# Performance work log

Hardware: AMD Instinct MI355X
Metric: run time of the kernel (lower is better)

Reference implementation:

```python
import jax, jax.numpy as jnp
import numpy as np

B, N, O, K, F = 4, 256, 5, 5, 256
H, D, DFF = 4, 64, 1024  # num_heads, KQ_len, FFN hidden
EPS = 1e-5


def setup_inputs() -> dict:
    key = jax.random.key(0)
    ks = jax.random.split(key, 16)
    s = 0.05
    p = lambda k, shape: (jax.random.normal(k, shape, jnp.float32) * s)
    return {
        "x": jax.random.normal(ks[0], (B, N, O, K, K, F), jnp.float32),
        "Wq": p(ks[1], (H * D, F)), "bq": p(ks[2], (H * D,)),
        "Wk": p(ks[3], (H * D, F)), "bk": p(ks[4], (H * D,)),
        "Wv": p(ks[5], (H * D, F)), "bv": p(ks[6], (H * D,)),
        "Wf": p(ks[7], (F, F)), "bf": p(ks[8], (F,)),
        "ln1_w": jnp.ones((N, O, F), jnp.float32), "ln1_b": jnp.zeros((N, O, F), jnp.float32),
        "ln2_w": jnp.ones((N, O, F), jnp.float32), "ln2_b": jnp.zeros((N, O, F), jnp.float32),
        "W1": p(ks[9], (DFF, F)), "b1": p(ks[10], (DFF,)),
        "W2": p(ks[11], (F, DFF)), "b2": p(ks[12], (F,)),
    }


def _layer_norm3(x, w, b):
    # torch LayerNorm with normalized_shape=[N, O, F]: stats over last 3 dims
    mu = jnp.mean(x, axis=(1, 2, 3), keepdims=True)
    var = jnp.var(x, axis=(1, 2, 3), keepdims=True)
    return (x - mu) * jax.lax.rsqrt(var + EPS) * w + b


def _split_heads(y):
    # [B,N,O,K,K,H*D] -> [B,N,O,H,K,K,D]
    return y.reshape(B, N, O, K, K, H, D).transpose(0, 1, 2, 5, 3, 4, 6)


def reference(x, Wq, bq, Wk, bk, Wv, bv, Wf, bf,
              ln1_w, ln1_b, ln2_w, ln2_b, W1, b1, W2, b2):
    q = _split_heads(x @ Wq.T + bq)
    k = _split_heads(x @ Wk.T + bk)
    v = _split_heads(x @ Wv.T + bv)
    c = K // 2
    qc = q[:, :, :, :, c, c, :]  # center query [B,N,O,H,D]
    # tile+mul+sum == dot of center query against every patch key
    scores = jnp.einsum('bnohd,bnohijd->bnohij', qc, k) / np.sqrt(float(D))
    w = jax.nn.softmax(scores.reshape(B, N, O, H, K * K), axis=-1)
    merged = jnp.einsum('bnohp,bnohpd->bnohd', w, v.reshape(B, N, O, H, K * K, D))
    merged = merged.reshape(B, N, O, H * D)
    attent = merged @ Wf.T + bf  # dropout = identity (eval)
    out1 = _layer_norm3(attent, ln1_w, ln1_b)
    ffn = jax.nn.relu(out1 @ W1.T + b1) @ W2.T + b2
    return _layer_norm3(out1 + ffn, ln2_w, ln2_b)
```

## Files before the change

kernel.cpp:

```cpp
#include <hip/hip_runtime.h>
#include <hip/hip_bf16.h>

#define FF 256
#define HH 4
#define DD 64
#define PP 25
#define SITES 5120
#define SPB 1280
#define DFF 1024
#define LN_ELEMS 327680

typedef const __hip_bfloat16* bfp;
typedef __hip_bfloat16* bfw;
typedef __attribute__((ext_vector_type(8))) short bf16x8;
typedef __attribute__((ext_vector_type(4))) float f32x4;

__device__ __forceinline__ float b2f(const __hip_bfloat16 v) { return __bfloat162float(v); }
__device__ __forceinline__ bool detect_bf(const unsigned* dt) {
    return dt[0] == 0x3F803F80u;
}
__device__ __forceinline__ float ldin(const void* p, size_t i, bool bf) {
    return bf ? __bfloat162float(((const __hip_bfloat16*)p)[i]) : ((const float*)p)[i];
}
__device__ __forceinline__ unsigned short f2bu(float f) {
    __hip_bfloat16 h = __float2bfloat16(f);
    return *(unsigned short*)&h;
}
__device__ __forceinline__ uint4 ldin8(const void* p, size_t i, bool bf) {
    if (bf) return *(const uint4*)((const unsigned short*)p + i);
    const float* f = (const float*)p + i;
    const float4 a = *(const float4*)f;
    const float4 b = *(const float4*)(f + 4);
    unsigned short u[8] = { f2bu(a.x), f2bu(a.y), f2bu(a.z), f2bu(a.w),
                            f2bu(b.x), f2bu(b.y), f2bu(b.z), f2bu(b.w) };
    return *(uint4*)u;
}

template<int RELU, int RES, int GATHER, int STATS, int BINT>
__global__ __launch_bounds__(256) void gemm_mfma(
    const void* xg, bfp Ab, int lda,
    const void* Bm, int ldb, const void* bias,
    bfp resid, int ldr, bfw C, int ldc, int Kc,
    int aoh, size_t boh, int bioh, int coh,
    float* __restrict__ red, const unsigned* dt)
{
    const bool bf = detect_bf(dt);
    const int h = blockIdx.z;
    Ab += (size_t)h * aoh;
    const size_t boff = (size_t)h * boh;
    const size_t biasoff = (size_t)h * bioh;
    C += (size_t)h * coh;

    __shared__ unsigned short Als[64][72];
    __shared__ unsigned short Bls[64][72];
    __shared__ float rs4[4], rss4[4];
    const int tid = threadIdx.x;
    const int lane = tid & 63;
    const int w = tid >> 6;
    const int m0 = blockIdx.y * 64;
    const int n0 = blockIdx.x * 64;
    const int r8 = tid >> 3;
    const int c8 = (tid & 7) * 8;

    f32x4 acc[4];
    #pragma unroll
    for (int mi = 0; mi < 4; ++mi) acc[mi] = (f32x4){0.f, 0.f, 0.f, 0.f};

    for (int k0 = 0; k0 < Kc; k0 += 64) {
        #pragma unroll
        for (int rr = 0; rr < 2; ++rr) {
            const int row = r8 + rr * 32;
            uint4 v;
            if (GATHER) v = ldin8(xg, ((size_t)(m0 + row) * PP + 12) * FF + (k0 + c8), bf);
            else        v = *(const uint4*)(Ab + (size_t)(m0 + row) * lda + (k0 + c8));
            *(uint4*)&Als[row][c8] = v;
        }
        #pragma unroll
        for (int rr = 0; rr < 2; ++rr) {
            const int row = r8 + rr * 32;
            const size_t bi = boff + (size_t)(n0 + row) * ldb + (k0 + c8);
            uint4 v;
            if (BINT) v = *(const uint4*)((const unsigned short*)Bm + bi);
            else      v = ldin8(Bm, bi, bf);
            *(uint4*)&Bls[row][c8] = v;
        }
        __syncthreads();
        #pragma unroll
        for (int ks = 0; ks < 2; ++ks) {
            const int kq = ks * 32 + (lane >> 4) * 8;
            const bf16x8 bfr = *(const bf16x8*)&Bls[w * 16 + (lane & 15)][kq];
            #pragma unroll
            for (int mi = 0; mi < 4; ++mi) {
                const bf16x8 afr = *(const bf16x8*)&Als[mi * 16 + (lane & 15)][kq];
                acc[mi] = __builtin_amdgcn_mfma_f32_16x16x32_bf16(afr, bfr, acc[mi], 0, 0, 0);
            }
        }
        __syncthreads();
    }

    const int col = n0 + w * 16 + (lane & 15);
    const int quad = lane >> 4;
    const float bvv = bias ? ldin(bias, biasoff + col, bf) : 0.f;
    float s_ = 0.f, ss_ = 0.f;
    #pragma unroll
    for (int mi = 0; mi < 4; ++mi) {
        #pragma unroll
        for (int r = 0; r < 4; ++r) {
            const int row = m0 + mi * 16 + quad * 4 + r;
            float v = acc[mi][r] + bvv;
            if (RES)  v += b2f(resid[(size_t)row * ldr + col]);
            if (RELU) v = fmaxf(v, 0.0f);
            if (STATS) { s_ += v; ss_ += v * v; }
            C[(size_t)row * ldc + col] = __float2bfloat16(v);
        }
    }
    if (STATS) {
        #pragma unroll
        for (int o = 32; o > 0; o >>= 1) { s_ += __shfl_down(s_, o); ss_ += __shfl_down(ss_, o); }
        if (lane == 0) { rs4[w] = s_; rss4[w] = ss_; }
        __syncthreads();
        if (tid == 0) {
            const int batch = m0 / SPB;
            atomicAdd(&red[batch * 2 + 0], rs4[0] + rs4[1] + rs4[2] + rs4[3]);
            atomicAdd(&red[batch * 2 + 1], rss4[0] + rss4[1] + rss4[2] + rss4[3]);
        }
    }
}

__global__ __launch_bounds__(256) void wkT_k(const void* Wk, bfw WkT, const unsigned* dt)
{
    const bool bf = detect_bf(dt);
    const int idx = blockIdx.x * 256 + threadIdx.x;
    const int d = idx & 63;
    const int f = (idx >> 6) & 255;
    const int h = idx >> 14;
    WkT[idx] = __float2bfloat16(ldin(Wk, (size_t)(h * DD + d) * FF + f, bf));
}

__global__ __launch_bounds__(256) void attn_site(const void* x, bfp qk, bfw xw,
                                                 const unsigned* dt)
{
    __shared__ unsigned short xsb[32][264];
    __shared__ unsigned short qkb[HH][FF];
    __shared__ float sc[HH][32];
    __shared__ float wl[HH][PP];

    const bool bf = detect_bf(dt);
    const int s = blockIdx.x;
    const int t = threadIdx.x;

    const size_t xbase = (size_t)s * (PP * FF);
    for (int e0 = t * 8; e0 < PP * FF; e0 += 2048)
        *(uint4*)&xsb[e0 >> 8][e0 & 255] = ldin8(x, xbase + e0, bf);
    if (t < 128)
        ((uint4*)qkb)[t] = ((const uint4*)(qk + (size_t)s * (HH * FF)))[t];
    __syncthreads();

    if (t < 64) {
        const int lane = t;
        const int col = lane & 15;
        const int quad = lane >> 4;
        const int brow = col & 3;
        f32x4 a0v = (f32x4){0.f, 0.f, 0.f, 0.f};
        f32x4 a1v = (f32x4){0.f, 0.f, 0.f, 0.f};
        #pragma unroll
        for (int ks = 0; ks < 8; ++ks) {
            const int kq = ks * 32 + quad * 8;
            const bf16x8 bfr = *(const bf16x8*)&qkb[brow][kq];
            const bf16x8 af0 = *(const bf16x8*)&xsb[col][kq];
            const bf16x8 af1 = *(const bf16x8*)&xsb[16 + col][kq];
            a0v = __builtin_amdgcn_mfma_f32_16x16x32_bf16(af0, bfr, a0v, 0, 0, 0);
            a1v = __builtin_amdgcn_mfma_f32_16x16x32_bf16(af1, bfr, a1v, 0, 0, 0);
        }
        if (col < HH) {
            #pragma unroll
            for (int r = 0; r < 4; ++r) {
                const int p = quad * 4 + r;
                sc[col][p] = a0v[r] * 0.125f;
                const int p2 = 16 + p;
                if (p2 < PP) sc[col][p2] = a1v[r] * 0.125f;
            }
        }
    }
    __syncthreads();

    if (t < HH) {
        float m = -1e30f;
        #pragma unroll
        for (int p = 0; p < PP; ++p) m = fmaxf(m, sc[t][p]);
        float e[PP], ssum = 0.f;
        #pragma unroll
        for (int p = 0; p < PP; ++p) { e[p] = __expf(sc[t][p] - m); ssum += e[p]; }
        const float inv = 1.f / ssum;
        #pragma unroll
        for (int p = 0; p < PP; ++p) wl[t][p] = e[p] * inv;
    }
    __syncthreads();

    float a0 = 0.f, a1 = 0.f, a2 = 0.f, a3 = 0.f;
    #pragma unroll
    for (int p = 0; p < PP; ++p) {
        const float xv = __bfloat162float(*(const __hip_bfloat16*)&xsb[p][t]);
        a0 = fmaf(wl[0][p], xv, a0);
        a1 = fmaf(wl[1][p], xv, a1);
        a2 = fmaf(wl[2][p], xv, a2);
        a3 = fmaf(wl[3][p], xv, a3);
    }
    bfw xwp = xw + (size_t)s * (HH * FF) + t;
    xwp[0 * FF] = __float2bfloat16(a0);
    xwp[1 * FF] = __float2bfloat16(a1);
    xwp[2 * FF] = __float2bfloat16(a2);
    xwp[3 * FF] = __float2bfloat16(a3);
}

template<int FINAL>
__global__ __launch_bounds__(256) void ln_apply(bfp X, const float* __restrict__ red,
                                                const void* w, const void* b,
                                                void* out, const unsigned* dt)
{
    const bool bf = detect_bf(dt);
    const int i8 = (blockIdx.x * 256 + threadIdx.x) * 8;
    const int s = i8 >> 8;
    const int batch = s / SPB;
    const int r = s - batch * SPB;
    const int f = i8 & 255;
    const float inv = 1.f / (float)LN_ELEMS;
    const float mu = red[batch * 2] * inv;
    const float var = red[batch * 2 + 1] * inv - mu * mu;
    const float rs = rsqrtf(var + 1e-5f);

    const uint4 xv = *(const uint4*)(X + i8);
    const uint4 wv = ldin8(w, (size_t)r * FF + f, bf);
    const uint4 bv = ldin8(b, (size_t)r * FF + f, bf);
    const unsigned short* xu = (const unsigned short*)&xv;
    const unsigned short* wu = (const unsigned short*)&wv;
    const unsigned short* bu = (const unsigned short*)&bv;
    float vo[8];
    #pragma unroll
    for (int j = 0; j < 8; ++j) {
        const float xf = __bfloat162float(*(const __hip_bfloat16*)&xu[j]);
        const float wf = __bfloat162float(*(const __hip_bfloat16*)&wu[j]);
        const float bf2 = __bfloat162float(*(const __hip_bfloat16*)&bu[j]);
        vo[j] = (xf - mu) * rs * wf + bf2;
    }
    if (FINAL && !bf) {
        float* o = (float*)out + i8;
        *(float4*)o = (float4){vo[0], vo[1], vo[2], vo[3]};
        *(float4*)(o + 4) = (float4){vo[4], vo[5], vo[6], vo[7]};
    } else {
        unsigned short ou[8];
        #pragma unroll
        for (int j = 0; j < 8; ++j) ou[j] = f2bu(vo[j]);
        *(uint4*)((unsigned short*)out + i8) = *(uint4*)ou;
    }
}

extern "C" void kernel_launch(void* const* d_in, const int* in_sizes, int n_in,
                              void* d_out, int out_size, void* d_ws, size_t ws_size,
                              hipStream_t stream)
{
    const void* x    = d_in[0];
    const void* Wq   = d_in[1];
    const void* bq   = d_in[2];
    const void* Wk   = d_in[3];
    const void* Wv   = d_in[5];
    const void* bv   = d_in[6];
    const void* Wf   = d_in[7];
    const void* bfv  = d_in[8];
    const void* ln1w = d_in[9];
    const void* ln1b = d_in[10];
    const void* ln2w = d_in[11];
    const void* ln2b = d_in[12];
    const void* W1   = d_in[13];
    const void* b1   = d_in[14];
    const void* W2   = d_in[15];
    const void* b2   = d_in[16];
    const unsigned* dt = (const unsigned*)d_in[9];

    char* w8 = (char*)d_ws;
    bfw qk   = (bfw)(w8);
    bfw xw   = (bfw)(w8 + 10485760);
    bfw hid  = (bfw)(w8 + 20971520);
    bfw WkT  = (bfw)(w8 + 31457280);
    bfw qc   = (bfw)(w8 + 32505856);
    bfw att  = (bfw)(w8 + 35127296);
    bfw out1 = (bfw)(w8 + 37748736);
    bfw z    = (bfw)(w8 + 40370176);
    float* red = (float*)(w8 + 42991616);

    hipMemsetAsync(red, 0, 64, stream);

    wkT_k<<<1024, 256, 0, stream>>>(Wk, WkT, dt);

    gemm_mfma<0, 0, 1, 0, 0><<<dim3(4, 80), 256, 0, stream>>>(
        x, nullptr, 0, Wq, FF, bq, nullptr, 0, qc, FF, FF, 0, 0, 0, 0, nullptr, dt);

    gemm_mfma<0, 0, 0, 0, 1><<<dim3(4, 80, HH), 256, 0, stream>>>(
        nullptr, qc, FF, WkT, DD, nullptr, nullptr, 0, qk, HH * FF, DD,
        DD, (size_t)FF * DD, 0, FF, nullptr, dt);

    attn_site<<<SITES, 256, 0, stream>>>(x, qk, xw, dt);

    gemm_mfma<0, 0, 0, 0, 0><<<dim3(1, 80, HH), 256, 0, stream>>>(
        nullptr, xw, HH * FF, Wv, FF, bv, nullptr, 0, qc, FF, FF,
        FF, (size_t)DD * FF, DD, DD, nullptr, dt);

    gemm_mfma<0, 0, 0, 1, 0><<<dim3(4, 80), 256, 0, stream>>>(
        nullptr, qc, FF, Wf, FF, bfv, nullptr, 0, att, FF, FF,
        0, 0, 0, 0, red, dt);

    ln_apply<0><<<640, 256, 0, stream>>>(att, red, ln1w, ln1b, out1, dt);

    gemm_mfma<1, 0, 0, 0, 0><<<dim3(16, 80), 256, 0, stream>>>(
        nullptr, out1, FF, W1, FF, b1, nullptr, 0, hid, DFF, FF,
        0, 0, 0, 0, nullptr, dt);

    gemm_mfma<0, 1, 0, 1, 0><<<dim3(4, 80), 256, 0, stream>>>(
        nullptr, hid, DFF, W2, DFF, b2, out1, FF, z, FF, DFF,
        0, 0, 0, 0, red + 8, dt);

    ln_apply<1><<<640, 256, 0, stream>>>(z, red + 8, ln2w, ln2b, d_out, dt);
}
```

Before: 335.7 us.

## Precompose Q·K and V·F weight products, fuse LN1 into FFN GEMMs

A prep kernel precomputes Wk^T·Wq per head (Qeff) with a folded query bias, and Wf·Wv (Weff) with a folded bias. The query-key projection becomes a single GEMM from the gathered center patch, and the value plus output projections collapse into one K=1024 GEMM. The LN1 apply kernel is removed: normalization is applied while loading the A operand of the W1 GEMM and recomputed in the W2 GEMM residual epilogue. This removes several launches and intermediate round trips. In exchange the value-output GEMM has a larger K, the prep kernel recomputes the weight products on every call, and the changed bf16 rounding points may shift accuracy.

Measured after the change: 379.8 us. 13.1% more time.

```diff
diff --git a/kernel.cpp b/kernel.cpp
--- a/kernel.cpp
+++ b/kernel.cpp
@@ -35,22 +35,75 @@
                             f2bu(b.x), f2bu(b.y), f2bu(b.z), f2bu(b.w) };
     return *(uint4*)u;
 }
-
-template<int RELU, int RES, int GATHER, int STATS, int BINT>
+__device__ __forceinline__ void ldin8v(const void* p, size_t i, bool bf, float* o) {
+    if (bf) {
+        const uint4 v = *(const uint4*)((const unsigned short*)p + i);
+        const unsigned short* u = (const unsigned short*)&v;
+        #pragma unroll
+        for (int j = 0; j < 8; ++j) o[j] = __bfloat162float(*(const __hip_bfloat16*)&u[j]);
+    } else {
+        const float4 a = *(const float4*)((const float*)p + i);
+        const float4 b = *(const float4*)((const float*)p + i + 4);
+        o[0]=a.x; o[1]=a.y; o[2]=a.z; o[3]=a.w; o[4]=b.x; o[5]=b.y; o[6]=b.z; o[7]=b.w;
+    }
+}
+
+__global__ __launch_bounds__(256) void prep_k(
+    const void* Wq, const void* bq, const void* Wk,
+    const void* Wv, const void* bv, const void* Wf, const void* bfv,
+    bfw Qeff, float* qb, bfw Weff, float* beff, const unsigned* dt)
+{
+    const bool bf = detect_bf(dt);
+    const int b = blockIdx.x;
+    const int t = threadIdx.x;
+    if (b < 1024) {
+        const int h = b >> 8, f = b & 255;
+        __shared__ float wkcol[DD];
+        if (t < DD) wkcol[t] = ldin(Wk, (size_t)(h * DD + t) * FF + f, bf);
+        __syncthreads();
+        float acc = 0.f;
+        #pragma unroll 8
+        for (int d = 0; d < DD; ++d)
+            acc = fmaf(wkcol[d], ldin(Wq, (size_t)(h * DD + d) * FF + t, bf), acc);
+        Qeff[(size_t)b * FF + t] = __float2bfloat16(acc);
+        if (t == 0) {
+            float a = 0.f;
+            #pragma unroll 8
+            for (int d = 0; d < DD; ++d) a = fmaf(ldin(bq, h * DD + d, bf), wkcol[d], a);
+            qb[b] = a;
+        }
+    } else {
+        const int j = b - 1024;
+        __shared__ float wfrow[FF];
+        wfrow[t] = ldin(Wf, (size_t)j * FF + t, bf);
+        __syncthreads();
+        #pragma unroll
+        for (int h = 0; h < HH; ++h) {
+            float acc = 0.f;
+            #pragma unroll 8
+            for (int d = 0; d < DD; ++d)
+                acc = fmaf(wfrow[h * DD + d], ldin(Wv, (size_t)(h * DD + d) * FF + t, bf), acc);
+            Weff[(size_t)j * DFF + h * FF + t] = __float2bfloat16(acc);
+        }
+        if (t == 0) {
+            float a = ldin(bfv, j, bf);
+            #pragma unroll 8
+            for (int i = 0; i < FF; ++i) a = fmaf(wfrow[i], ldin(bv, i, bf), a);
+            beff[j] = a;
+        }
+    }
+}
+
+template<int RELU, int RESMODE, int GATHER, int STATS, int BINT, int BIASF, int LNA>
 __global__ __launch_bounds__(256) void gemm_mfma(
-    const void* xg, bfp Ab, int lda,
+    const void* Ag, int lda,
     const void* Bm, int ldb, const void* bias,
-    bfp resid, int ldr, bfw C, int ldc, int Kc,
-    int aoh, size_t boh, int bioh, int coh,
-    float* __restrict__ red, const unsigned* dt)
+    const void* resid, int ldr,
+    bfw C, int ldc, int Kc,
+    const float* lnred, const void* lnw, const void* lnb,
+    float* red_out, const unsigned* dt)
 {
     const bool bf = detect_bf(dt);
-    const int h = blockIdx.z;
-    Ab += (size_t)h * aoh;
-    const size_t boff = (size_t)h * boh;
-    const size_t biasoff = (size_t)h * bioh;
-    C += (size_t)h * coh;
-
     __shared__ unsigned short Als[64][72];
     __shared__ unsigned short Bls[64][72];
     __shared__ float rs4[4], rss4[4];
@@ -62,6 +115,15 @@
     const int r8 = tid >> 3;
     const int c8 = (tid & 7) * 8;
 
+    const int batch_ = m0 / SPB;
+    float mu_ = 0.f, rsc_ = 0.f;
+    if (LNA || RESMODE == 2) {
+        const float inv = 1.f / (float)LN_ELEMS;
+        mu_ = lnred[batch_ * 2] * inv;
+        const float var = lnred[batch_ * 2 + 1] * inv - mu_ * mu_;
+        rsc_ = rsqrtf(var + 1e-5f);
+    }
+
     f32x4 acc[4];
     #pragma unroll
     for (int mi = 0; mi < 4; ++mi) acc[mi] = (f32x4){0.f, 0.f, 0.f, 0.f};
@@ -70,15 +132,33 @@
         #pragma unroll
         for (int rr = 0; rr < 2; ++rr) {
             const int row = r8 + rr * 32;
+            const int grow = m0 + row;
             uint4 v;
-            if (GATHER) v = ldin8(xg, ((size_t)(m0 + row) * PP + 12) * FF + (k0 + c8), bf);
-            else        v = *(const uint4*)(Ab + (size_t)(m0 + row) * lda + (k0 + c8));
+            if (GATHER) {
+                v = ldin8(Ag, ((size_t)grow * PP + 12) * FF + (k0 + c8), bf);
+            } else if (LNA) {
+                const int r_ = grow - batch_ * SPB;
+                const uint4 av = *(const uint4*)((const unsigned short*)Ag + (size_t)grow * lda + k0 + c8);
+                const unsigned short* au = (const unsigned short*)&av;
+                float wv8[8], bv8[8];
+                ldin8v(lnw, (size_t)r_ * FF + k0 + c8, bf, wv8);
+                ldin8v(lnb, (size_t)r_ * FF + k0 + c8, bf, bv8);
+                unsigned short o[8];
+                #pragma unroll
+                for (int j = 0; j < 8; ++j) {
+                    const float xf = __bfloat162float(*(const __hip_bfloat16*)&au[j]);
+                    o[j] = f2bu((xf - mu_) * rsc_ * wv8[j] + bv8[j]);
+                }
+                v = *(uint4*)o;
+            } else {
+                v = *(const uint4*)((const unsigned short*)Ag + (size_t)grow * lda + k0 + c8);
+            }
             *(uint4*)&Als[row][c8] = v;
         }
         #pragma unroll
         for (int rr = 0; rr < 2; ++rr) {
             const int row = r8 + rr * 32;
-            const size_t bi = boff + (size_t)(n0 + row) * ldb + (k0 + c8);
+            const size_t bi = (size_t)(n0 + row) * ldb + (k0 + c8);
             uint4 v;
             if (BINT) v = *(const uint4*)((const unsigned short*)Bm + bi);
             else      v = ldin8(Bm, bi, bf);
@@ -100,7 +180,8 @@
 
     const int col = n0 + w * 16 + (lane & 15);
     const int quad = lane >> 4;
-    const float bvv = bias ? ldin(bias, biasoff + col, bf) : 0.f;
+    float bvv = 0.f;
+    if (bias) bvv = BIASF ? ((const float*)bias)[col] : ldin(bias, col, bf);
     float s_ = 0.f, ss_ = 0.f;
     #pragma unroll
     for (int mi = 0; mi < 4; ++mi) {
@@ -108,7 +189,12 @@
         for (int r = 0; r < 4; ++r) {
             const int row = m0 + mi * 16 + quad * 4 + r;
             float v = acc[mi][r] + bvv;
-            if (RES)  v += b2f(resid[(size_t)row * ldr + col]);
+            if (RESMODE == 2) {
+                const int r_ = row - batch_ * SPB;
+                const float af = b2f(((bfp)resid)[(size_t)row * ldr + col]);
+                v += (af - mu_) * rsc_ * ldin(lnw, (size_t)r_ * FF + col, bf)
+                     + ldin(lnb, (size_t)r_ * FF + col, bf);
+            }
             if (RELU) v = fmaxf(v, 0.0f);
             if (STATS) { s_ += v; ss_ += v * v; }
             C[(size_t)row * ldc + col] = __float2bfloat16(v);
@@ -120,21 +206,10 @@
         if (lane == 0) { rs4[w] = s_; rss4[w] = ss_; }
         __syncthreads();
         if (tid == 0) {
-            const int batch = m0 / SPB;
-            atomicAdd(&red[batch * 2 + 0], rs4[0] + rs4[1] + rs4[2] + rs4[3]);
-            atomicAdd(&red[batch * 2 + 1], rss4[0] + rss4[1] + rss4[2] + rss4[3]);
-        }
-    }
-}
-
-__global__ __launch_bounds__(256) void wkT_k(const void* Wk, bfw WkT, const unsigned* dt)
-{
-    const bool bf = detect_bf(dt);
-    const int idx = blockIdx.x * 256 + threadIdx.x;
-    const int d = idx & 63;
-    const int f = (idx >> 6) & 255;
-    const int h = idx >> 14;
-    WkT[idx] = __float2bfloat16(ldin(Wk, (size_t)(h * DD + d) * FF + f, bf));
+            atomicAdd(&red_out[batch_ * 2 + 0], rs4[0] + rs4[1] + rs4[2] + rs4[3]);
+            atomicAdd(&red_out[batch_ * 2 + 1], rss4[0] + rss4[1] + rss4[2] + rss4[3]);
+        }
+    }
 }
 
 __global__ __launch_bounds__(256) void attn_site(const void* x, bfp qk, bfw xw,
@@ -157,9 +232,8 @@
     __syncthreads();
 
     if (t < 64) {
-        const int lane = t;
-        const int col = lane & 15;
-        const int quad = lane >> 4;
+        const int col = t & 15;
+        const int quad = t >> 4;
         const int brow = col & 3;
         f32x4 a0v = (f32x4){0.f, 0.f, 0.f, 0.f};
         f32x4 a1v = (f32x4){0.f, 0.f, 0.f, 0.f};
@@ -213,8 +287,7 @@
     xwp[3 * FF] = __float2bfloat16(a3);
 }
 
-template<int FINAL>
-__global__ __launch_bounds__(256) void ln_apply(bfp X, const float* __restrict__ red,
+__global__ __launch_bounds__(256) void ln_final(bfp X, const float* __restrict__ red,
                                                 const void* w, const void* b,
                                                 void* out, const unsigned* dt)
 {
@@ -230,20 +303,16 @@
     const float rs = rsqrtf(var + 1e-5f);
 
     const uint4 xv = *(const uint4*)(X + i8);
-    const uint4 wv = ldin8(w, (size_t)r * FF + f, bf);
-    const uint4 bv = ldin8(b, (size_t)r * FF + f, bf);
     const unsigned short* xu = (const unsigned short*)&xv;
-    const unsigned short* wu = (const unsigned short*)&wv;
-    const unsigned short* bu = (const unsigned short*)&bv;
-    float vo[8];
+    float wv[8], bv[8], vo[8];
+    ldin8v(w, (size_t)r * FF + f, bf, wv);
+    ldin8v(b, (size_t)r * FF + f, bf, bv);
     #pragma unroll
     for (int j = 0; j < 8; ++j) {
         const float xf = __bfloat162float(*(const __hip_bfloat16*)&xu[j]);
-        const float wf = __bfloat162float(*(const __hip_bfloat16*)&wu[j]);
-        const float bf2 = __bfloat162float(*(const __hip_bfloat16*)&bu[j]);
-        vo[j] = (xf - mu) * rs * wf + bf2;
-    }
-    if (FINAL && !bf) {
+        vo[j] = (xf - mu) * rs * wv[j] + bv[j];
+    }
+    if (!bf) {
         float* o = (float*)out + i8;
         *(float4*)o = (float4){vo[0], vo[1], vo[2], vo[3]};
         *(float4*)(o + 4) = (float4){vo[4], vo[5], vo[6], vo[7]};
@@ -281,43 +350,36 @@
     bfw qk   = (bfw)(w8);
     bfw xw   = (bfw)(w8 + 10485760);
     bfw hid  = (bfw)(w8 + 20971520);
-    bfw WkT  = (bfw)(w8 + 31457280);
-    bfw qc   = (bfw)(w8 + 32505856);
-    bfw att  = (bfw)(w8 + 35127296);
-    bfw out1 = (bfw)(w8 + 37748736);
-    bfw z    = (bfw)(w8 + 40370176);
-    float* red = (float*)(w8 + 42991616);
+    bfw att  = (bfw)(w8 + 31457280);
+    bfw z    = (bfw)(w8 + 34078720);
+    bfw Qeff = (bfw)(w8 + 36700160);
+    bfw Weff = (bfw)(w8 + 37224448);
+    float* qb   = (float*)(w8 + 37748736);
+    float* beff = (float*)(w8 + 37752832);
+    float* red  = (float*)(w8 + 37753856);
 
     hipMemsetAsync(red, 0, 64, stream);
 
-    wkT_k<<<1024, 256, 0, stream>>>(Wk, WkT, dt);
-
-    gemm_mfma<0, 0, 1, 0, 0><<<dim3(4, 80), 256, 0, stream>>>(
-        x, nullptr, 0, Wq, FF, bq, nullptr, 0, qc, FF, FF, 0, 0, 0, 0, nullptr, dt);
-
-    gemm_mfma<0, 0, 0, 0, 1><<<dim3(4, 80, HH), 256, 0, stream>>>(
-        nullptr, qc, FF, WkT, DD, nullptr, nullptr, 0, qk, HH * FF, DD,
-        DD, (size_t)FF * DD, 0, FF, nullptr, dt);
+    prep_k<<<1280, 256, 0, stream>>>(Wq, bq, Wk, Wv, bv, Wf, bfv,
+                                     Qeff, qb, Weff, beff, dt);
+
+    gemm_mfma<0, 0, 1, 0, 1, 1, 0><<<dim3(16, 80), 256, 0, stream>>>(
+        x, 0, Qeff, FF, qb, nullptr, 0, qk, DFF, FF,
+        nullptr, nullptr, nullptr, nullptr, dt);
 
     attn_site<<<SITES, 256, 0, stream>>>(x, qk, xw, dt);
 
-    gemm_mfma<0, 0, 0, 0, 0><<<dim3(1, 80, HH), 256, 0, stream>>>(
-        nullptr, xw, HH * FF, Wv, FF, bv, nullptr, 0, qc, FF, FF,
-        FF, (size_t)DD * FF, DD, DD, nullptr, dt);
-
-    gemm_mfma<0, 0, 0, 1, 0><<<dim3(4, 80), 256, 0, stream>>>(
-        nullptr, qc, FF, Wf, FF, bfv, nullptr, 0, att, FF, FF,
-        0, 0, 0, 0, red, dt);
-
-    ln_apply<0><<<640, 256, 0, stream>>>(att, red, ln1w, ln1b, out1, dt);
-
-    gemm_mfma<1, 0, 0, 0, 0><<<dim3(16, 80), 256, 0, stream>>>(
-        nullptr, out1, FF, W1, FF, b1, nullptr, 0, hid, DFF, FF,
-        0, 0, 0, 0, nullptr, dt);
-
-    gemm_mfma<0, 1, 0, 1, 0><<<dim3(4, 80), 256, 0, stream>>>(
-        nullptr, hid, DFF, W2, DFF, b2, out1, FF, z, FF, DFF,
-        0, 0, 0, 0, red + 8, dt);
-
-    ln_apply<1><<<640, 256, 0, stream>>>(z, red + 8, ln2w, ln2b, d_out, dt);
-}
+    gemm_mfma<0, 0, 0, 1, 1, 1, 0><<<dim3(4, 80), 256, 0, stream>>>(
+        xw, DFF, Weff, DFF, beff, nullptr, 0, att, FF, DFF,
+        nullptr, nullptr, nullptr, red, dt);
+
+    gemm_mfma<1, 0, 0, 0, 0, 0, 1><<<dim3(16, 80), 256, 0, stream>>>(
+        att, FF, W1, FF, b1, nullptr, 0, hid, DFF, FF,
+        red, ln1w, ln1b, nullptr, dt);
+
+    gemm_mfma<0, 2, 0, 1, 0, 0, 0><<<dim3(4, 80), 256, 0, stream>>>(
+        hid, DFF, W2, DFF, b2, att, FF, z, FF, DFF,
+        red, ln1w, ln1b, red + 8, dt);
+
+    ln_final<<<640, 256, 0, stream>>>(z, red + 8, ln2w, ln2b, d_out, dt);
+}
```
